# Kernel tuning notes

Hardware: AMD Instinct MI355X
Metric: run time of the kernel (lower is better)

The kernel has to match this reference:

```python
import jax, jax.numpy as jnp
import numpy as np

D_MODEL = 2048
NUM_HEADS = 16
HEAD_DIM = 128
BATCH = 4
SEQ = 2048


def setup_inputs() -> dict:
    key = jax.random.key(0)
    ks = jax.random.split(key, 5)
    s = 0.02
    return {
        "x": jax.random.normal(ks[0], (BATCH, SEQ, D_MODEL), dtype=jnp.float32),
        "Wq": jax.random.normal(ks[1], (NUM_HEADS * HEAD_DIM, D_MODEL), dtype=jnp.float32) * s,
        "Wk": jax.random.normal(ks[2], (NUM_HEADS * HEAD_DIM, D_MODEL), dtype=jnp.float32) * s,
        "Wv": jax.random.normal(ks[3], (NUM_HEADS * HEAD_DIM, D_MODEL), dtype=jnp.float32) * s,
        "Wo": jax.random.normal(ks[4], (D_MODEL, NUM_HEADS * HEAD_DIM), dtype=jnp.float32) * s,
    }


def _split_heads(t):
    b, s, _ = t.shape
    return t.reshape(b, s, NUM_HEADS, HEAD_DIM).transpose(0, 2, 1, 3)  # [b,h,s,d]


def reference(x, Wq, Wk, Wv, Wo):
    # prefill: QKV proj + causal SDPA + output proj. torch Linear: x @ W.T
    q = _split_heads(x @ Wq.T)
    k = _split_heads(x @ Wk.T)
    v = _split_heads(x @ Wv.T)
    scale = 1.0 / jnp.sqrt(jnp.asarray(HEAD_DIM, dtype=x.dtype))
    scores = jnp.einsum("bhqd,bhkd->bhqk", q, k) * scale
    causal = jnp.tril(jnp.ones((SEQ, SEQ), dtype=bool))
    scores = jnp.where(causal, scores, jnp.finfo(scores.dtype).min)
    attn = jax.nn.softmax(scores, axis=-1)
    y = jnp.einsum("bhqk,bhkd->bhqd", attn, v)
    y = y.transpose(0, 2, 1, 3).reshape(x.shape[0], SEQ, NUM_HEADS * HEAD_DIM)
    y = y @ Wo.T
    return (y, k, v)
```

## Files before the change

### kernel.cpp

```cpp
#include <hip/hip_runtime.h>
#include <stdint.h>

#define DM 2048
#define NH 16
#define HD 128
#define BB 4
#define SS 2048
#define BS (BB*SS)
#define NQKV (3*DM)
#define SCQ 0.12751744565f

typedef __bf16 bf16_t;
typedef __attribute__((ext_vector_type(8))) __bf16 bf16x8;
typedef __attribute__((ext_vector_type(4))) float f32x4;
typedef __attribute__((ext_vector_type(16))) float f32x16;
typedef __attribute__((ext_vector_type(4))) float float4v;
typedef __attribute__((ext_vector_type(4))) unsigned int uint4v;
typedef __attribute__((ext_vector_type(4))) unsigned short ushort4v;
typedef __attribute__((ext_vector_type(8))) unsigned short ushort8;

__device__ __forceinline__ unsigned short f2bf(float f) {
  unsigned u = __float_as_uint(f);
  u += 0x7fffu + ((u >> 16) & 1u);
  return (unsigned short)(u >> 16);
}

__device__ __forceinline__ void gl16(const void* g, void* l) {
  __builtin_amdgcn_global_load_lds(
      (const __attribute__((address_space(1))) unsigned int*)(unsigned long long)g,
      (__attribute__((address_space(3))) unsigned int*)(unsigned int)(unsigned long long)l,
      16, 0, 0);
}

__global__ void conv_f32_bf16(const float* __restrict__ in,
                              unsigned short* __restrict__ out, int n4) {
  int i = blockIdx.x * blockDim.x + threadIdx.x;
  int stride = gridDim.x * blockDim.x;
  for (; i < n4; i += stride) {
    float4v v = ((const float4v*)in)[i];
    ushort4v o;
    o.x = f2bf(v.x); o.y = f2bf(v.y); o.z = f2bf(v.z); o.w = f2bf(v.w);
    ((ushort4v*)out)[i] = o;
  }
}

template<int MODE>
__global__ __launch_bounds__(512)
void gemm256(const bf16_t* __restrict__ A, const bf16_t* __restrict__ Bm,
             const int K, const int N, const int nbx,
             float* __restrict__ Cf, bf16_t* __restrict__ qbf,
             bf16_t* __restrict__ kbt, float* __restrict__ kf,
             float* __restrict__ vf, bf16_t* __restrict__ vtb) {
  __shared__ bf16_t As[4][256 * 32];
  __shared__ bf16_t Bs[4][256 * 32];
  const int t = threadIdx.x, w = t >> 6, lane = t & 63;
  const int fr = lane & 15, fq = lane >> 4;
  const int cpx = gridDim.x >> 3;
  const int orig = blockIdx.x;
  const int wg = (orig & 7) * cpx + (orig >> 3);
  const int bm = wg % nbx, bn = wg / nbx;
  const int row0 = bm * 256, col0 = bn * 256;
  const int wm = (w >> 2) * 128, wn = (w & 3) * 64;

  const int i0 = t, i1 = 512 + t;
  const int r0 = i0 >> 2, c0 = i0 & 3;
  const int r1 = i1 >> 2, c1 = i1 & 3;
  const bf16_t* A0 = A + (size_t)(row0 + r0) * K + ((c0 ^ ((r0 >> 1) & 3)) * 8);
  const bf16_t* A1 = A + (size_t)(row0 + r1) * K + ((c1 ^ ((r1 >> 1) & 3)) * 8);
  const bf16_t* B0 = Bm + (size_t)(col0 + r0) * K + ((c0 ^ ((r0 >> 1) & 3)) * 8);
  const bf16_t* B1 = Bm + (size_t)(col0 + r1) * K + ((c1 ^ ((r1 >> 1) & 3)) * 8);

  const int NT = K >> 5;
  f32x4 acc[8][4] = {};

#define STAGE(TT)                                                      \
  {                                                                    \
    const int sl_ = (TT) & 3;                                          \
    const size_t ko_ = (size_t)(TT) * 32;                              \
    gl16(A0 + ko_, (char*)(&As[sl_][0]) + w * 1024);                   \
    gl16(A1 + ko_, (char*)(&As[sl_][0]) + 8192 + w * 1024);            \
    gl16(B0 + ko_, (char*)(&Bs[sl_][0]) + w * 1024);                   \
    gl16(B1 + ko_, (char*)(&Bs[sl_][0]) + 8192 + w * 1024);            \
  }

  STAGE(0); STAGE(1); STAGE(2);

  for (int T = 0; T < NT; ++T) {
    if (T + 3 < NT) {
      STAGE(T + 3);
      asm volatile("s_waitcnt vmcnt(12)" ::: "memory");
    } else if (T + 3 == NT) {
      asm volatile("s_waitcnt vmcnt(8)" ::: "memory");
    } else if (T + 2 == NT) {
      asm volatile("s_waitcnt vmcnt(4)" ::: "memory");
    } else {
      asm volatile("s_waitcnt vmcnt(0)" ::: "memory");
    }
    asm volatile("s_barrier" ::: "memory");

    const bf16_t* al = &As[T & 3][0];
    const bf16_t* bl = &Bs[T & 3][0];
    bf16x8 bfv[4];
#pragma unroll
    for (int n = 0; n < 4; ++n) {
      int rb = wn + n * 16 + fr;
      bfv[n] = *(const bf16x8*)(bl + rb * 32 + ((fq ^ ((rb >> 1) & 3)) * 8));
    }
    __builtin_amdgcn_s_setprio(1);
#pragma unroll
    for (int f = 0; f < 8; ++f) {
      int ra = wm + f * 16 + fr;
      bf16x8 af = *(const bf16x8*)(al + ra * 32 + ((fq ^ ((ra >> 1) & 3)) * 8));
#pragma unroll
      for (int n = 0; n < 4; ++n)
        acc[f][n] = __builtin_amdgcn_mfma_f32_16x16x32_bf16(af, bfv[n], acc[f][n], 0, 0, 0);
    }
    __builtin_amdgcn_s_setprio(0);
    asm volatile("s_barrier" ::: "memory");
  }
#undef STAGE

#pragma unroll
  for (int f = 0; f < 8; ++f) {
#pragma unroll
    for (int jn = 0; jn < 4; ++jn) {
#pragma unroll
      for (int r = 0; r < 4; ++r) {
        int m = row0 + wm + f * 16 + fq * 4 + r;
        int n = col0 + wn + jn * 16 + fr;
        float v = acc[f][jn][r];
        if (MODE == 0) {
          Cf[(size_t)m * N + n] = v;
        } else {
          int b = m >> 11, s = m & 2047;
          if (n < DM) {
            int h = n >> 7, d = n & 127;
            qbf[(((size_t)(b * NH + h)) * SS + s) * HD + d] = (bf16_t)(v * SCQ);
          } else if (n < 2 * DM) {
            int nn = n - DM, h = nn >> 7, d = nn & 127;
            size_t o = (((size_t)(b * NH + h)) * SS + s) * HD + d;
            kbt[o] = (bf16_t)v;
            kf[o] = v;
          } else {
            int nn = n - 2 * DM, h = nn >> 7, d = nn & 127;
            size_t o = (((size_t)(b * NH + h)) * SS + s) * HD + d;
            vf[o] = v;
            vtb[((size_t)(b * NH + h)) * (HD * SS) + (size_t)d * SS + s] = (bf16_t)v;
          }
        }
      }
    }
  }
}

__global__ __launch_bounds__(256, 2)
void attn_fwd4(const bf16_t* __restrict__ qbf, const bf16_t* __restrict__ kbf,
               const bf16_t* __restrict__ vt, bf16_t* __restrict__ aout) {
  __shared__ bf16_t Ks[2][64 * 128];
  __shared__ bf16_t Vs[2][64 * 128];
  const int t = threadIdx.x, w = t >> 6, lane = t & 63;
  const int l31 = lane & 31, hi = lane >> 5;
  const int orig = blockIdx.x;
  const int wg = (orig & 7) * 128 + (orig >> 3);
  const int bh = wg >> 4;
  const int qt = 15 - (wg & 15);
  const int q0 = qt * 128;
  const int nt = 2 * qt + 2;
  const size_t bh_off = (size_t)bh * SS * HD;
  const char* kbase = (const char*)(kbf + bh_off);
  const char* vbase = (const char*)(vt + bh_off);

  const char* ksrc[4];
  const char* vsrc[4];
#pragma unroll
  for (int i = 0; i < 4; ++i) {
    int r = (w * 4 + i) * 4 + (lane >> 4);
    int c = (lane & 15) ^ (r & 15);
    ksrc[i] = kbase + r * 256 + c * 16;
    int d = 2 * r + (c >> 3);
    vsrc[i] = vbase + (size_t)d * (SS * 2) + (c & 7) * 16;
  }

  bf16x8 qfr[8];
  {
    const char* qrow = (const char*)(qbf + bh_off + (size_t)(q0 + w * 32 + l31) * HD);
#pragma unroll
    for (int ds = 0; ds < 8; ++ds)
      qfr[ds] = *(const bf16x8*)(qrow + ds * 32 + hi * 16);
  }

#pragma unroll
  for (int i = 0; i < 4; ++i) {
    gl16(ksrc[i], (char*)(&Ks[0][0]) + (w * 4 + i) * 1024);
    gl16(vsrc[i], (char*)(&Vs[0][0]) + (w * 4 + i) * 1024);
    ksrc[i] += 16384;
    vsrc[i] += 128;
  }

  float mrow = -3.0e38f, lrow = 0.f;
  f32x16 accO[4] = {};

  auto make_pa = [&](const f32x16& sv, bf16x8& paA, bf16x8& paB) {
    unsigned W[8];
#pragma unroll
    for (int m = 0; m < 8; ++m) {
      float lo = sv[2 * m], hh = sv[2 * m + 1];
      asm("v_cvt_pk_bf16_f32 %0, %1, %2" : "=v"(W[m]) : "v"(lo), "v"(hh));
    }
#pragma unroll
    for (int g = 0; g < 2; ++g) {
      unsigned A = W[4 * g], B = W[4 * g + 1], C = W[4 * g + 2], D = W[4 * g + 3];
      unsigned xA = (unsigned)__shfl_xor((int)A, 32, 64);
      unsigned xB = (unsigned)__shfl_xor((int)B, 32, 64);
      unsigned xC = (unsigned)__shfl_xor((int)C, 32, 64);
      unsigned xD = (unsigned)__shfl_xor((int)D, 32, 64);
      uint4v u;
      u.x = hi ? xC : A;
      u.y = hi ? xD : B;
      u.z = hi ? C : xA;
      u.w = hi ? D : xB;
      if (g == 0) paA = __builtin_bit_cast(bf16x8, u);
      else        paB = __builtin_bit_cast(bf16x8, u);
    }
  };

  for (int kt = 0; kt < nt; ++kt) {
    const int cur = kt & 1;
    __syncthreads();

    if (kt + 1 < nt) {
#pragma unroll
      for (int i = 0; i < 4; ++i) {
        gl16(ksrc[i], (char*)(&Ks[cur ^ 1][0]) + (w * 4 + i) * 1024);
        gl16(vsrc[i], (char*)(&Vs[cur ^ 1][0]) + (w * 4 + i) * 1024);
        ksrc[i] += 16384;
        vsrc[i] += 128;
      }
    }

    const char* kl = (const char*)&Ks[cur][0];
    f32x16 s0 = {}, s1 = {};
    const int rck = l31 & 15;
    __builtin_amdgcn_s_setprio(1);
#pragma unroll
    for (int ds = 0; ds < 8; ++ds) {
      int ch = ((2 * ds + hi) ^ rck) << 4;
      bf16x8 kf0 = *(const bf16x8*)(kl + l31 * 256 + ch);
      s0 = __builtin_amdgcn_mfma_f32_32x32x16_bf16(kf0, qfr[ds], s0, 0, 0, 0);
      bf16x8 kf1 = *(const bf16x8*)(kl + (32 + l31) * 256 + ch);
      s1 = __builtin_amdgcn_mfma_f32_32x32x16_bf16(kf1, qfr[ds], s1, 0, 0, 0);
    }
    __builtin_amdgcn_s_setprio(0);

    const int kv0 = kt * 64;
    if (kt >= 2 * qt) {
      const int qg = q0 + w * 32 + l31;
#pragma unroll
      for (int r = 0; r < 16; ++r) {
        int klo = kv0 + (r & 3) + 8 * (r >> 2) + 4 * hi;
        if (klo > qg) s0[r] = -3.0e38f;
        if (klo + 32 > qg) s1[r] = -3.0e38f;
      }
    }
    float rm = s0[0];
#pragma unroll
    for (int r = 1; r < 16; ++r) rm = fmaxf(rm, s0[r]);
#pragma unroll
    for (int r = 0; r < 16; ++r) rm = fmaxf(rm, s1[r]);
    rm = fmaxf(rm, __shfl_xor(rm, 32, 64));
    if (__ballot(rm > mrow + 8.0f)) {
      float mnew = fmaxf(mrow, rm);
      float fct = __builtin_amdgcn_exp2f(mrow - mnew);
      mrow = mnew;
      lrow *= fct;
#pragma unroll
      for (int r = 0; r < 16; ++r) {
        float f = __shfl(fct, (r & 3) + 8 * (r >> 2) + 4 * hi, 64);
        accO[0][r] *= f; accO[1][r] *= f; accO[2][r] *= f; accO[3][r] *= f;
      }
    }
    float ss = 0.f;
#pragma unroll
    for (int r = 0; r < 16; ++r) { float p = __builtin_amdgcn_exp2f(s0[r] - mrow); s0[r] = p; ss += p; }
#pragma unroll
    for (int r = 0; r < 16; ++r) { float p = __builtin_amdgcn_exp2f(s1[r] - mrow); s1[r] = p; ss += p; }
    ss += __shfl_xor(ss, 32, 64);
    lrow += ss;

    bf16x8 pa00, pa01, pa10, pa11;
    make_pa(s0, pa00, pa01);
    make_pa(s1, pa10, pa11);

    const char* vl = (const char*)&Vs[cur][0];
    __builtin_amdgcn_s_setprio(1);
#pragma unroll
    for (int dt = 0; dt < 4; ++dt) {
      int R = dt * 16 + (l31 >> 1);
      int cb = (l31 & 1) << 3;
      int rx = R & 15;
      bf16x8 v00 = *(const bf16x8*)(vl + R * 256 + (((cb + 0 + hi) ^ rx) << 4));
      accO[dt] = __builtin_amdgcn_mfma_f32_32x32x16_bf16(pa00, v00, accO[dt], 0, 0, 0);
      bf16x8 v01 = *(const bf16x8*)(vl + R * 256 + (((cb + 2 + hi) ^ rx) << 4));
      accO[dt] = __builtin_amdgcn_mfma_f32_32x32x16_bf16(pa01, v01, accO[dt], 0, 0, 0);
      bf16x8 v10 = *(const bf16x8*)(vl + R * 256 + (((cb + 4 + hi) ^ rx) << 4));
      accO[dt] = __builtin_amdgcn_mfma_f32_32x32x16_bf16(pa10, v10, accO[dt], 0, 0, 0);
      bf16x8 v11 = *(const bf16x8*)(vl + R * 256 + (((cb + 6 + hi) ^ rx) << 4));
      accO[dt] = __builtin_amdgcn_mfma_f32_32x32x16_bf16(pa11, v11, accO[dt], 0, 0, 0);
    }
    __builtin_amdgcn_s_setprio(0);
  }

  const int b = bh >> 4, h = bh & 15;
#pragma unroll
  for (int r = 0; r < 16; ++r) {
    int qr = (r & 3) + 8 * (r >> 2) + 4 * hi;
    float inv = __builtin_amdgcn_rcpf(__shfl(lrow, qr, 64));
    int srow = q0 + w * 32 + qr;
    bf16_t* orow = aout + ((size_t)(b * SS + srow)) * DM + h * HD + l31;
    orow[0]  = (bf16_t)(accO[0][r] * inv);
    orow[32] = (bf16_t)(accO[1][r] * inv);
    orow[64] = (bf16_t)(accO[2][r] * inv);
    orow[96] = (bf16_t)(accO[3][r] * inv);
  }
}

extern "C" void kernel_launch(void* const* d_in, const int* in_sizes, int n_in,
                              void* d_out, int out_size, void* d_ws, size_t ws_size,
                              hipStream_t stream) {
  (void)in_sizes; (void)n_in; (void)out_size; (void)ws_size;
  const float* x  = (const float*)d_in[0];
  const float* Wq = (const float*)d_in[1];
  const float* Wk = (const float*)d_in[2];
  const float* Wv = (const float*)d_in[3];
  const float* Wo = (const float*)d_in[4];

  float* y  = (float*)d_out;
  float* kf = y + (size_t)BS * DM;
  float* vf = kf + (size_t)BS * DM;

  char* ws = (char*)d_ws;
  bf16_t* xbf  = (bf16_t*)ws;
  bf16_t* abf  = xbf;
  bf16_t* qbf  = (bf16_t*)(ws + (size_t)32 * 1024 * 1024);
  bf16_t* wobf = qbf;
  bf16_t* wqkv = (bf16_t*)(ws + (size_t)64 * 1024 * 1024);
  bf16_t* kbt  = (bf16_t*)y;
  bf16_t* vtb  = (bf16_t*)((char*)y + (size_t)32 * 1024 * 1024);

  conv_f32_bf16<<<2048, 256, 0, stream>>>(x, (unsigned short*)xbf, BS * DM / 4);
  conv_f32_bf16<<<512, 256, 0, stream>>>(Wq, (unsigned short*)wqkv, DM * DM / 4);
  conv_f32_bf16<<<512, 256, 0, stream>>>(Wk, (unsigned short*)(wqkv + (size_t)DM * DM), DM * DM / 4);
  conv_f32_bf16<<<512, 256, 0, stream>>>(Wv, (unsigned short*)(wqkv + 2 * (size_t)DM * DM), DM * DM / 4);

  gemm256<1><<<768, 512, 0, stream>>>(
      xbf, wqkv, DM, NQKV, 32, nullptr, qbf, kbt, kf, vf, vtb);

  attn_fwd4<<<1024, 256, 0, stream>>>(qbf, kbt, vtb, abf);

  conv_f32_bf16<<<512, 256, 0, stream>>>(Wo, (unsigned short*)wobf, DM * DM / 4);

  gemm256<0><<<256, 512, 0, stream>>>(
      abf, wobf, DM, DM, 32, y, nullptr, nullptr, nullptr, nullptr, nullptr);
}
```

Before: 529.3 us.

## Restructure GEMM into double-buffered K=64 tiles with ping-pong barrier phases

Replaces the 4-stage, K=32 LDS pipeline of the 256x256 GEMM with a 2-buffer, K=64 pipeline using an 8-row XOR swizzle. The main loop is split into four sub-phases separated by barriers, and the B-tile prefetch is deferred to the second phase. This aims to halve the outer-loop barrier count per K and interleave warp scheduling, ping-pong style, so loads overlap MFMA work. LDS use stays at 128KB, but prefetch depth drops to a single stage, so memory latency may be less well hidden.

```diff
diff --git a/kernel.cpp b/kernel.cpp
--- a/kernel.cpp
+++ b/kernel.cpp
@@ -46,13 +46,13 @@
 
 template<int MODE>
 __global__ __launch_bounds__(512)
-void gemm256(const bf16_t* __restrict__ A, const bf16_t* __restrict__ Bm,
-             const int K, const int N, const int nbx,
-             float* __restrict__ Cf, bf16_t* __restrict__ qbf,
-             bf16_t* __restrict__ kbt, float* __restrict__ kf,
-             float* __restrict__ vf, bf16_t* __restrict__ vtb) {
-  __shared__ bf16_t As[4][256 * 32];
-  __shared__ bf16_t Bs[4][256 * 32];
+void gemm8p(const bf16_t* __restrict__ A, const bf16_t* __restrict__ Bm,
+            const int K, const int N, const int nbx,
+            float* __restrict__ Cf, bf16_t* __restrict__ qbf,
+            bf16_t* __restrict__ kbt, float* __restrict__ kf,
+            float* __restrict__ vf, bf16_t* __restrict__ vtb) {
+  __shared__ bf16_t As[2][256 * 64];
+  __shared__ bf16_t Bs[2][256 * 64];
   const int t = threadIdx.x, w = t >> 6, lane = t & 63;
   const int fr = lane & 15, fq = lane >> 4;
   const int cpx = gridDim.x >> 3;
@@ -62,63 +62,126 @@
   const int row0 = bm * 256, col0 = bn * 256;
   const int wm = (w >> 2) * 128, wn = (w & 3) * 64;
 
-  const int i0 = t, i1 = 512 + t;
-  const int r0 = i0 >> 2, c0 = i0 & 3;
-  const int r1 = i1 >> 2, c1 = i1 & 3;
-  const bf16_t* A0 = A + (size_t)(row0 + r0) * K + ((c0 ^ ((r0 >> 1) & 3)) * 8);
-  const bf16_t* A1 = A + (size_t)(row0 + r1) * K + ((c1 ^ ((r1 >> 1) & 3)) * 8);
-  const bf16_t* B0 = Bm + (size_t)(col0 + r0) * K + ((c0 ^ ((r0 >> 1) & 3)) * 8);
-  const bf16_t* B1 = Bm + (size_t)(col0 + r1) * K + ((c1 ^ ((r1 >> 1) & 3)) * 8);
-
-  const int NT = K >> 5;
+  const bf16_t* Asrc[4];
+  const bf16_t* Bsrc[4];
+  int dst[4];
+#pragma unroll
+  for (int j = 0; j < 4; ++j) {
+    int u = j * 512 + t, r = u >> 3, c = u & 7;
+    Asrc[j] = A + (size_t)(row0 + r) * K + ((c ^ (r & 7)) * 8);
+    Bsrc[j] = Bm + (size_t)(col0 + r) * K + ((c ^ (r & 7)) * 8);
+    dst[j] = u * 16;
+  }
+  const int NT = K >> 6;
   f32x4 acc[8][4] = {};
 
-#define STAGE(TT)                                                      \
-  {                                                                    \
-    const int sl_ = (TT) & 3;                                          \
-    const size_t ko_ = (size_t)(TT) * 32;                              \
-    gl16(A0 + ko_, (char*)(&As[sl_][0]) + w * 1024);                   \
-    gl16(A1 + ko_, (char*)(&As[sl_][0]) + 8192 + w * 1024);            \
-    gl16(B0 + ko_, (char*)(&Bs[sl_][0]) + w * 1024);                   \
-    gl16(B1 + ko_, (char*)(&Bs[sl_][0]) + 8192 + w * 1024);            \
-  }
-
-  STAGE(0); STAGE(1); STAGE(2);
+#pragma unroll
+  for (int j = 0; j < 4; ++j) gl16(Asrc[j], (char*)(&As[0][0]) + dst[j]);
+#pragma unroll
+  for (int j = 0; j < 4; ++j) gl16(Bsrc[j], (char*)(&Bs[0][0]) + dst[j]);
 
   for (int T = 0; T < NT; ++T) {
-    if (T + 3 < NT) {
-      STAGE(T + 3);
-      asm volatile("s_waitcnt vmcnt(12)" ::: "memory");
-    } else if (T + 3 == NT) {
-      asm volatile("s_waitcnt vmcnt(8)" ::: "memory");
-    } else if (T + 2 == NT) {
+    const bf16_t* al = &As[T & 1][0];
+    const bf16_t* bl = &Bs[T & 1][0];
+    char* Ad = (char*)(&As[(T & 1) ^ 1][0]);
+    char* Bd = (char*)(&Bs[(T & 1) ^ 1][0]);
+    const size_t ko = (size_t)(T + 1) * 64;
+
+    if (T + 1 < NT) {
+#pragma unroll
+      for (int j = 0; j < 4; ++j) gl16(Asrc[j] + ko, Ad + dst[j]);
       asm volatile("s_waitcnt vmcnt(4)" ::: "memory");
     } else {
       asm volatile("s_waitcnt vmcnt(0)" ::: "memory");
     }
     asm volatile("s_barrier" ::: "memory");
 
-    const bf16_t* al = &As[T & 3][0];
-    const bf16_t* bl = &Bs[T & 3][0];
-    bf16x8 bfv[4];
+    auto LDA = [&](int f, int ks) {
+      int ra = wm + f * 16 + fr;
+      return *(const bf16x8*)(al + ra * 64 + (((fq + ks * 4) ^ (ra & 7)) * 8));
+    };
+
+    bf16x8 bfv[4][2];
 #pragma unroll
     for (int n = 0; n < 4; ++n) {
       int rb = wn + n * 16 + fr;
-      bfv[n] = *(const bf16x8*)(bl + rb * 32 + ((fq ^ ((rb >> 1) & 3)) * 8));
-    }
-    __builtin_amdgcn_s_setprio(1);
-#pragma unroll
-    for (int f = 0; f < 8; ++f) {
-      int ra = wm + f * 16 + fr;
-      bf16x8 af = *(const bf16x8*)(al + ra * 32 + ((fq ^ ((ra >> 1) & 3)) * 8));
-#pragma unroll
-      for (int n = 0; n < 4; ++n)
-        acc[f][n] = __builtin_amdgcn_mfma_f32_16x16x32_bf16(af, bfv[n], acc[f][n], 0, 0, 0);
-    }
-    __builtin_amdgcn_s_setprio(0);
-    asm volatile("s_barrier" ::: "memory");
-  }
-#undef STAGE
+#pragma unroll
+      for (int ks = 0; ks < 2; ++ks)
+        bfv[n][ks] = *(const bf16x8*)(bl + rb * 64 + (((fq + ks * 4) ^ (rb & 7)) * 8));
+    }
+    {
+      bf16x8 a00 = LDA(0, 0), a01 = LDA(0, 1), a10 = LDA(1, 0), a11 = LDA(1, 1);
+      __builtin_amdgcn_s_barrier();
+      __builtin_amdgcn_s_setprio(1);
+#pragma unroll
+      for (int n = 0; n < 4; ++n) {
+        acc[0][n] = __builtin_amdgcn_mfma_f32_16x16x32_bf16(a00, bfv[n][0], acc[0][n], 0, 0, 0);
+        acc[1][n] = __builtin_amdgcn_mfma_f32_16x16x32_bf16(a10, bfv[n][0], acc[1][n], 0, 0, 0);
+      }
+#pragma unroll
+      for (int n = 0; n < 4; ++n) {
+        acc[0][n] = __builtin_amdgcn_mfma_f32_16x16x32_bf16(a01, bfv[n][1], acc[0][n], 0, 0, 0);
+        acc[1][n] = __builtin_amdgcn_mfma_f32_16x16x32_bf16(a11, bfv[n][1], acc[1][n], 0, 0, 0);
+      }
+      __builtin_amdgcn_s_setprio(0);
+      __builtin_amdgcn_s_barrier();
+    }
+    {
+      bf16x8 a00 = LDA(2, 0), a01 = LDA(2, 1), a10 = LDA(3, 0), a11 = LDA(3, 1);
+      if (T + 1 < NT) {
+#pragma unroll
+        for (int j = 0; j < 4; ++j) gl16(Bsrc[j] + ko, Bd + dst[j]);
+      }
+      __builtin_amdgcn_s_barrier();
+      __builtin_amdgcn_s_setprio(1);
+#pragma unroll
+      for (int n = 0; n < 4; ++n) {
+        acc[2][n] = __builtin_amdgcn_mfma_f32_16x16x32_bf16(a00, bfv[n][0], acc[2][n], 0, 0, 0);
+        acc[3][n] = __builtin_amdgcn_mfma_f32_16x16x32_bf16(a10, bfv[n][0], acc[3][n], 0, 0, 0);
+      }
+#pragma unroll
+      for (int n = 0; n < 4; ++n) {
+        acc[2][n] = __builtin_amdgcn_mfma_f32_16x16x32_bf16(a01, bfv[n][1], acc[2][n], 0, 0, 0);
+        acc[3][n] = __builtin_amdgcn_mfma_f32_16x16x32_bf16(a11, bfv[n][1], acc[3][n], 0, 0, 0);
+      }
+      __builtin_amdgcn_s_setprio(0);
+      __builtin_amdgcn_s_barrier();
+    }
+    {
+      bf16x8 a00 = LDA(4, 0), a01 = LDA(4, 1), a10 = LDA(5, 0), a11 = LDA(5, 1);
+      __builtin_amdgcn_s_barrier();
+      __builtin_amdgcn_s_setprio(1);
+#pragma unroll
+      for (int n = 0; n < 4; ++n) {
+        acc[4][n] = __builtin_amdgcn_mfma_f32_16x16x32_bf16(a00, bfv[n][0], acc[4][n], 0, 0, 0);
+        acc[5][n] = __builtin_amdgcn_mfma_f32_16x16x32_bf16(a10, bfv[n][0], acc[5][n], 0, 0, 0);
+      }
+#pragma unroll
+      for (int n = 0; n < 4; ++n) {
+        acc[4][n] = __builtin_amdgcn_mfma_f32_16x16x32_bf16(a01, bfv[n][1], acc[4][n], 0, 0, 0);
+        acc[5][n] = __builtin_amdgcn_mfma_f32_16x16x32_bf16(a11, bfv[n][1], acc[5][n], 0, 0, 0);
+      }
+      __builtin_amdgcn_s_setprio(0);
+      __builtin_amdgcn_s_barrier();
+    }
+    {
+      bf16x8 a00 = LDA(6, 0), a01 = LDA(6, 1), a10 = LDA(7, 0), a11 = LDA(7, 1);
+      __builtin_amdgcn_s_barrier();
+      __builtin_amdgcn_s_setprio(1);
+#pragma unroll
+      for (int n = 0; n < 4; ++n) {
+        acc[6][n] = __builtin_amdgcn_mfma_f32_16x16x32_bf16(a00, bfv[n][0], acc[6][n], 0, 0, 0);
+        acc[7][n] = __builtin_amdgcn_mfma_f32_16x16x32_bf16(a10, bfv[n][0], acc[7][n], 0, 0, 0);
+      }
+#pragma unroll
+      for (int n = 0; n < 4; ++n) {
+        acc[6][n] = __builtin_amdgcn_mfma_f32_16x16x32_bf16(a01, bfv[n][1], acc[6][n], 0, 0, 0);
+        acc[7][n] = __builtin_amdgcn_mfma_f32_16x16x32_bf16(a11, bfv[n][1], acc[7][n], 0, 0, 0);
+      }
+      __builtin_amdgcn_s_setprio(0);
+      __builtin_amdgcn_s_barrier();
+    }
+  }
 
 #pragma unroll
   for (int f = 0; f < 8; ++f) {
@@ -352,13 +415,13 @@
   conv_f32_bf16<<<512, 256, 0, stream>>>(Wk, (unsigned short*)(wqkv + (size_t)DM * DM), DM * DM / 4);
   conv_f32_bf16<<<512, 256, 0, stream>>>(Wv, (unsigned short*)(wqkv + 2 * (size_t)DM * DM), DM * DM / 4);
 
-  gemm256<1><<<768, 512, 0, stream>>>(
+  gemm8p<1><<<768, 512, 0, stream>>>(
       xbf, wqkv, DM, NQKV, 32, nullptr, qbf, kbt, kf, vf, vtb);
 
   attn_fwd4<<<1024, 256, 0, stream>>>(qbf, kbt, vtb, abf);
 
   conv_f32_bf16<<<512, 256, 0, stream>>>(Wo, (unsigned short*)wobf, DM * DM / 4);
 
-  gemm256<0><<<256, 512, 0, stream>>>(
+  gemm8p<0><<<256, 512, 0, stream>>>(
       abf, wobf, DM, DM, 32, y, nullptr, nullptr, nullptr, nullptr, nullptr);
 }
```

Measured after the change: 510.3 us. 1.04x faster.

## Restructure GEMM to 64-deep K tiles with double buffering and interleaved phases

Applied to the files above, without the earlier changes.

Replaces the 4-stage, K=32 LDS pipeline in both GEMMs with a 2-stage, K=64 double buffer. The global-to-LDS loads for the next tile are split across MFMA phases, and LDS reads are issued as inline ds_read_b128 with immediate offsets under an 8-way XOR swizzle. The aim is fewer barriers per unit of K, global loads that overlap compute, and less address arithmetic. In exchange it adds more barriers per iteration and has only one tile of prefetch depth, so global latency may be exposed.

```diff
diff --git a/kernel.cpp b/kernel.cpp
--- a/kernel.cpp
+++ b/kernel.cpp
@@ -31,6 +31,9 @@
       (__attribute__((address_space(3))) unsigned int*)(unsigned int)(unsigned long long)l,
       16, 0, 0);
 }
+
+#define DSR(dst, addr, IMM)                                                   \
+  asm volatile("ds_read_b128 %0, %1 offset:" IMM : "=v"(dst) : "v"(addr))
 
 __global__ void conv_f32_bf16(const float* __restrict__ in,
                               unsigned short* __restrict__ out, int n4) {
@@ -46,13 +49,13 @@
 
 template<int MODE>
 __global__ __launch_bounds__(512)
-void gemm256(const bf16_t* __restrict__ A, const bf16_t* __restrict__ Bm,
-             const int K, const int N, const int nbx,
-             float* __restrict__ Cf, bf16_t* __restrict__ qbf,
-             bf16_t* __restrict__ kbt, float* __restrict__ kf,
-             float* __restrict__ vf, bf16_t* __restrict__ vtb) {
-  __shared__ bf16_t As[4][256 * 32];
-  __shared__ bf16_t Bs[4][256 * 32];
+void gemm8a(const bf16_t* __restrict__ A, const bf16_t* __restrict__ Bm,
+            const int K, const int N, const int nbx,
+            float* __restrict__ Cf, bf16_t* __restrict__ qbf,
+            bf16_t* __restrict__ kbt, float* __restrict__ kf,
+            float* __restrict__ vf, bf16_t* __restrict__ vtb) {
+  __shared__ bf16_t As[2][256 * 64];
+  __shared__ bf16_t Bs[2][256 * 64];
   const int t = threadIdx.x, w = t >> 6, lane = t & 63;
   const int fr = lane & 15, fq = lane >> 4;
   const int cpx = gridDim.x >> 3;
@@ -62,63 +65,109 @@
   const int row0 = bm * 256, col0 = bn * 256;
   const int wm = (w >> 2) * 128, wn = (w & 3) * 64;
 
-  const int i0 = t, i1 = 512 + t;
-  const int r0 = i0 >> 2, c0 = i0 & 3;
-  const int r1 = i1 >> 2, c1 = i1 & 3;
-  const bf16_t* A0 = A + (size_t)(row0 + r0) * K + ((c0 ^ ((r0 >> 1) & 3)) * 8);
-  const bf16_t* A1 = A + (size_t)(row0 + r1) * K + ((c1 ^ ((r1 >> 1) & 3)) * 8);
-  const bf16_t* B0 = Bm + (size_t)(col0 + r0) * K + ((c0 ^ ((r0 >> 1) & 3)) * 8);
-  const bf16_t* B1 = Bm + (size_t)(col0 + r1) * K + ((c1 ^ ((r1 >> 1) & 3)) * 8);
-
-  const int NT = K >> 5;
+  const bf16_t* Asrc[4];
+  const bf16_t* Bsrc[4];
+  int dst[4];
+#pragma unroll
+  for (int j = 0; j < 4; ++j) {
+    int u = j * 512 + t, r = u >> 3, c = u & 7;
+    Asrc[j] = A + (size_t)(row0 + r) * K + ((c ^ (r & 7)) * 8);
+    Bsrc[j] = Bm + (size_t)(col0 + r) * K + ((c ^ (r & 7)) * 8);
+    dst[j] = u * 16;
+  }
+  const int NT = K >> 6;
   f32x4 acc[8][4] = {};
 
-#define STAGE(TT)                                                      \
-  {                                                                    \
-    const int sl_ = (TT) & 3;                                          \
-    const size_t ko_ = (size_t)(TT) * 32;                              \
-    gl16(A0 + ko_, (char*)(&As[sl_][0]) + w * 1024);                   \
-    gl16(A1 + ko_, (char*)(&As[sl_][0]) + 8192 + w * 1024);            \
-    gl16(B0 + ko_, (char*)(&Bs[sl_][0]) + w * 1024);                   \
-    gl16(B1 + ko_, (char*)(&Bs[sl_][0]) + 8192 + w * 1024);            \
-  }
-
-  STAGE(0); STAGE(1); STAGE(2);
+  const unsigned As0 = (unsigned)(unsigned long long)(const void*)&As[0][0];
+  const unsigned Bs0 = (unsigned)(unsigned long long)(const void*)&Bs[0][0];
+  const unsigned arow = (unsigned)(wm + fr) * 128;
+  const unsigned brow = (unsigned)(wn + fr) * 128;
+  const unsigned x0 = (unsigned)((fq ^ (fr & 7)) * 16);
+  const unsigned x1 = (unsigned)(((fq + 4) ^ (fr & 7)) * 16);
+
+#pragma unroll
+  for (int j = 0; j < 4; ++j) gl16(Asrc[j], (char*)(&As[0][0]) + dst[j]);
+#pragma unroll
+  for (int j = 0; j < 4; ++j) gl16(Bsrc[j], (char*)(&Bs[0][0]) + dst[j]);
+  asm volatile("s_waitcnt vmcnt(0)" ::: "memory");
+  asm volatile("s_barrier" ::: "memory");
+
+#define MFMA_PAIR(F0, F1)                                                     \
+  __builtin_amdgcn_s_setprio(1);                                              \
+  _Pragma("unroll")                                                           \
+  for (int n = 0; n < 4; ++n) {                                               \
+    acc[F0][n] = __builtin_amdgcn_mfma_f32_16x16x32_bf16(                     \
+        __builtin_bit_cast(bf16x8, q00), __builtin_bit_cast(bf16x8, bfv[n][0]), acc[F0][n], 0, 0, 0); \
+    acc[F1][n] = __builtin_amdgcn_mfma_f32_16x16x32_bf16(                     \
+        __builtin_bit_cast(bf16x8, q10), __builtin_bit_cast(bf16x8, bfv[n][0]), acc[F1][n], 0, 0, 0); \
+  }                                                                           \
+  _Pragma("unroll")                                                           \
+  for (int n = 0; n < 4; ++n) {                                               \
+    acc[F0][n] = __builtin_amdgcn_mfma_f32_16x16x32_bf16(                     \
+        __builtin_bit_cast(bf16x8, q01), __builtin_bit_cast(bf16x8, bfv[n][1]), acc[F0][n], 0, 0, 0); \
+    acc[F1][n] = __builtin_amdgcn_mfma_f32_16x16x32_bf16(                     \
+        __builtin_bit_cast(bf16x8, q11), __builtin_bit_cast(bf16x8, bfv[n][1]), acc[F1][n], 0, 0, 0); \
+  }                                                                           \
+  __builtin_amdgcn_s_setprio(0);
 
   for (int T = 0; T < NT; ++T) {
-    if (T + 3 < NT) {
-      STAGE(T + 3);
-      asm volatile("s_waitcnt vmcnt(12)" ::: "memory");
-    } else if (T + 3 == NT) {
-      asm volatile("s_waitcnt vmcnt(8)" ::: "memory");
-    } else if (T + 2 == NT) {
-      asm volatile("s_waitcnt vmcnt(4)" ::: "memory");
-    } else {
-      asm volatile("s_waitcnt vmcnt(0)" ::: "memory");
-    }
-    asm volatile("s_barrier" ::: "memory");
-
-    const bf16_t* al = &As[T & 3][0];
-    const bf16_t* bl = &Bs[T & 3][0];
-    bf16x8 bfv[4];
-#pragma unroll
-    for (int n = 0; n < 4; ++n) {
-      int rb = wn + n * 16 + fr;
-      bfv[n] = *(const bf16x8*)(bl + rb * 32 + ((fq ^ ((rb >> 1) & 3)) * 8));
-    }
-    __builtin_amdgcn_s_setprio(1);
-#pragma unroll
-    for (int f = 0; f < 8; ++f) {
-      int ra = wm + f * 16 + fr;
-      bf16x8 af = *(const bf16x8*)(al + ra * 32 + ((fq ^ ((ra >> 1) & 3)) * 8));
-#pragma unroll
-      for (int n = 0; n < 4; ++n)
-        acc[f][n] = __builtin_amdgcn_mfma_f32_16x16x32_bf16(af, bfv[n], acc[f][n], 0, 0, 0);
-    }
-    __builtin_amdgcn_s_setprio(0);
-    asm volatile("s_barrier" ::: "memory");
-  }
-#undef STAGE
+    char* Ad = (char*)(&As[(T & 1) ^ 1][0]);
+    char* Bd = (char*)(&Bs[(T & 1) ^ 1][0]);
+    const size_t ko = (size_t)(T + 1) * 64;
+    const unsigned ab = As0 + (unsigned)(T & 1) * 32768;
+    const unsigned bb = Bs0 + (unsigned)(T & 1) * 32768;
+    const unsigned a0 = ab + arow + x0, a1 = ab + arow + x1;
+    const unsigned b0 = bb + brow + x0, b1 = bb + brow + x1;
+
+    uint4v bfv[4][2];
+    uint4v q00, q01, q10, q11;
+
+    DSR(bfv[0][0], b0, "0");    DSR(bfv[0][1], b1, "0");
+    DSR(bfv[1][0], b0, "2048"); DSR(bfv[1][1], b1, "2048");
+    DSR(bfv[2][0], b0, "4096"); DSR(bfv[2][1], b1, "4096");
+    DSR(bfv[3][0], b0, "6144"); DSR(bfv[3][1], b1, "6144");
+    DSR(q00, a0, "0");    DSR(q01, a1, "0");
+    DSR(q10, a0, "2048"); DSR(q11, a1, "2048");
+    if (T + 1 < NT) {
+#pragma unroll
+      for (int j = 0; j < 4; ++j) gl16(Asrc[j] + ko, Ad + dst[j]);
+    }
+    asm volatile("s_barrier" ::: "memory");
+    asm volatile("s_waitcnt lgkmcnt(0)" ::: "memory");
+    __builtin_amdgcn_sched_barrier(0);
+    MFMA_PAIR(0, 1)
+    asm volatile("s_barrier" ::: "memory");
+
+    DSR(q00, a0, "4096"); DSR(q01, a1, "4096");
+    DSR(q10, a0, "6144"); DSR(q11, a1, "6144");
+    if (T + 1 < NT) {
+#pragma unroll
+      for (int j = 0; j < 4; ++j) gl16(Bsrc[j] + ko, Bd + dst[j]);
+    }
+    asm volatile("s_barrier" ::: "memory");
+    asm volatile("s_waitcnt lgkmcnt(0)" ::: "memory");
+    __builtin_amdgcn_sched_barrier(0);
+    MFMA_PAIR(2, 3)
+    asm volatile("s_barrier" ::: "memory");
+
+    DSR(q00, a0, "8192");  DSR(q01, a1, "8192");
+    DSR(q10, a0, "10240"); DSR(q11, a1, "10240");
+    asm volatile("s_barrier" ::: "memory");
+    asm volatile("s_waitcnt lgkmcnt(0)" ::: "memory");
+    __builtin_amdgcn_sched_barrier(0);
+    MFMA_PAIR(4, 5)
+    asm volatile("s_barrier" ::: "memory");
+
+    DSR(q00, a0, "12288"); DSR(q01, a1, "12288");
+    DSR(q10, a0, "14336"); DSR(q11, a1, "14336");
+    asm volatile("s_barrier" ::: "memory");
+    asm volatile("s_waitcnt lgkmcnt(0)" ::: "memory");
+    __builtin_amdgcn_sched_barrier(0);
+    MFMA_PAIR(6, 7)
+    asm volatile("s_waitcnt vmcnt(0)" ::: "memory");
+    asm volatile("s_barrier" ::: "memory");
+  }
+#undef MFMA_PAIR
 
 #pragma unroll
   for (int f = 0; f < 8; ++f) {
@@ -352,13 +401,13 @@
   conv_f32_bf16<<<512, 256, 0, stream>>>(Wk, (unsigned short*)(wqkv + (size_t)DM * DM), DM * DM / 4);
   conv_f32_bf16<<<512, 256, 0, stream>>>(Wv, (unsigned short*)(wqkv + 2 * (size_t)DM * DM), DM * DM / 4);
 
-  gemm256<1><<<768, 512, 0, stream>>>(
+  gemm8a<1><<<768, 512, 0, stream>>>(
       xbf, wqkv, DM, NQKV, 32, nullptr, qbf, kbt, kf, vf, vtb);
 
   attn_fwd4<<<1024, 256, 0, stream>>>(qbf, kbt, vtb, abf);
 
   conv_f32_bf16<<<512, 256, 0, stream>>>(Wo, (unsigned short*)wobf, DM * DM / 4);
 
-  gemm256<0><<<256, 512, 0, stream>>>(
+  gemm8a<0><<<256, 512, 0, stream>>>(
       abf, wobf, DM, DM, 32, y, nullptr, nullptr, nullptr, nullptr, nullptr);
 }
```

Result: faster. 518.7 us (-2.0%).

## Restructure GEMM main loop: single barrier, batched LDS reads, split waits

Applied to the files above, without the earlier changes.

Reworks the bf16 GEMM inner loop so each K-step uses one barrier instead of two. The prefetch for stage T+3 is now issued after the barrier, into the slot that was consumed in the previous iteration. All LDS fragment reads are issued up front as inline ds_read_b128 with immediate offsets. The first half of the MFMAs starts after a partial lgkmcnt wait, which overlaps LDS latency with math. The swizzle pattern also changes to a simpler r&3 XOR. The aim is to cut barrier stalls and LDS address arithmetic, at the cost of fragile hand-written waitcnt bookkeeping.

```diff
diff --git a/kernel.cpp b/kernel.cpp
--- a/kernel.cpp
+++ b/kernel.cpp
@@ -31,6 +31,9 @@
       (__attribute__((address_space(3))) unsigned int*)(unsigned int)(unsigned long long)l,
       16, 0, 0);
 }
+
+#define DSR(dst, addr, IMM)                                                   \
+  asm volatile("ds_read_b128 %0, %1 offset:" IMM : "=v"(dst) : "v"(addr))
 
 __global__ void conv_f32_bf16(const float* __restrict__ in,
                               unsigned short* __restrict__ out, int n4) {
@@ -46,11 +49,11 @@
 
 template<int MODE>
 __global__ __launch_bounds__(512)
-void gemm256(const bf16_t* __restrict__ A, const bf16_t* __restrict__ Bm,
-             const int K, const int N, const int nbx,
-             float* __restrict__ Cf, bf16_t* __restrict__ qbf,
-             bf16_t* __restrict__ kbt, float* __restrict__ kf,
-             float* __restrict__ vf, bf16_t* __restrict__ vtb) {
+void gemmr4(const bf16_t* __restrict__ A, const bf16_t* __restrict__ Bm,
+            const int K, const int N, const int nbx,
+            float* __restrict__ Cf, bf16_t* __restrict__ qbf,
+            bf16_t* __restrict__ kbt, float* __restrict__ kf,
+            float* __restrict__ vf, bf16_t* __restrict__ vtb) {
   __shared__ bf16_t As[4][256 * 32];
   __shared__ bf16_t Bs[4][256 * 32];
   const int t = threadIdx.x, w = t >> 6, lane = t & 63;
@@ -62,63 +65,82 @@
   const int row0 = bm * 256, col0 = bn * 256;
   const int wm = (w >> 2) * 128, wn = (w & 3) * 64;
 
-  const int i0 = t, i1 = 512 + t;
-  const int r0 = i0 >> 2, c0 = i0 & 3;
-  const int r1 = i1 >> 2, c1 = i1 & 3;
-  const bf16_t* A0 = A + (size_t)(row0 + r0) * K + ((c0 ^ ((r0 >> 1) & 3)) * 8);
-  const bf16_t* A1 = A + (size_t)(row0 + r1) * K + ((c1 ^ ((r1 >> 1) & 3)) * 8);
-  const bf16_t* B0 = Bm + (size_t)(col0 + r0) * K + ((c0 ^ ((r0 >> 1) & 3)) * 8);
-  const bf16_t* B1 = Bm + (size_t)(col0 + r1) * K + ((c1 ^ ((r1 >> 1) & 3)) * 8);
-
+  const bf16_t* Asrc[2];
+  const bf16_t* Bsrc[2];
+  int dst[2];
+#pragma unroll
+  for (int j = 0; j < 2; ++j) {
+    int u = j * 512 + t, r = u >> 2, c = u & 3;
+    Asrc[j] = A + (size_t)(row0 + r) * K + ((c ^ (r & 3)) * 8);
+    Bsrc[j] = Bm + (size_t)(col0 + r) * K + ((c ^ (r & 3)) * 8);
+    dst[j] = u * 16;
+  }
   const int NT = K >> 5;
   f32x4 acc[8][4] = {};
 
-#define STAGE(TT)                                                      \
-  {                                                                    \
-    const int sl_ = (TT) & 3;                                          \
-    const size_t ko_ = (size_t)(TT) * 32;                              \
-    gl16(A0 + ko_, (char*)(&As[sl_][0]) + w * 1024);                   \
-    gl16(A1 + ko_, (char*)(&As[sl_][0]) + 8192 + w * 1024);            \
-    gl16(B0 + ko_, (char*)(&Bs[sl_][0]) + w * 1024);                   \
-    gl16(B1 + ko_, (char*)(&Bs[sl_][0]) + 8192 + w * 1024);            \
-  }
+  const unsigned As0 = (unsigned)(unsigned long long)(const void*)&As[0][0];
+  const unsigned Bs0 = (unsigned)(unsigned long long)(const void*)&Bs[0][0];
+  const unsigned xorc = (unsigned)((fq ^ (fr & 3)) << 4);
+  const unsigned aoff = (unsigned)((wm + fr) * 64) + xorc;
+  const unsigned boff = (unsigned)((wn + fr) * 64) + xorc;
+
+#define STAGE(TT)                                                  \
+  {                                                                \
+    const int sl_ = (TT) & 3;                                      \
+    const size_t ko_ = (size_t)(TT) * 32;                          \
+    gl16(Asrc[0] + ko_, (char*)(&As[sl_][0]) + dst[0]);            \
+    gl16(Asrc[1] + ko_, (char*)(&As[sl_][0]) + dst[1]);            \
+    gl16(Bsrc[0] + ko_, (char*)(&Bs[sl_][0]) + dst[0]);            \
+    gl16(Bsrc[1] + ko_, (char*)(&Bs[sl_][0]) + dst[1]);            \
+  }
+
+#define MFQUAD(FI, AV)                                                        \
+  acc[FI][0] = __builtin_amdgcn_mfma_f32_16x16x32_bf16(                       \
+      __builtin_bit_cast(bf16x8, AV), __builtin_bit_cast(bf16x8, bv0), acc[FI][0], 0, 0, 0); \
+  acc[FI][1] = __builtin_amdgcn_mfma_f32_16x16x32_bf16(                       \
+      __builtin_bit_cast(bf16x8, AV), __builtin_bit_cast(bf16x8, bv1), acc[FI][1], 0, 0, 0); \
+  acc[FI][2] = __builtin_amdgcn_mfma_f32_16x16x32_bf16(                       \
+      __builtin_bit_cast(bf16x8, AV), __builtin_bit_cast(bf16x8, bv2), acc[FI][2], 0, 0, 0); \
+  acc[FI][3] = __builtin_amdgcn_mfma_f32_16x16x32_bf16(                       \
+      __builtin_bit_cast(bf16x8, AV), __builtin_bit_cast(bf16x8, bv3), acc[FI][3], 0, 0, 0);
 
   STAGE(0); STAGE(1); STAGE(2);
 
   for (int T = 0; T < NT; ++T) {
-    if (T + 3 < NT) {
-      STAGE(T + 3);
-      asm volatile("s_waitcnt vmcnt(12)" ::: "memory");
-    } else if (T + 3 == NT) {
+    if (T + 2 < NT) {
       asm volatile("s_waitcnt vmcnt(8)" ::: "memory");
-    } else if (T + 2 == NT) {
+    } else if (T + 1 < NT) {
       asm volatile("s_waitcnt vmcnt(4)" ::: "memory");
     } else {
       asm volatile("s_waitcnt vmcnt(0)" ::: "memory");
     }
     asm volatile("s_barrier" ::: "memory");
-
-    const bf16_t* al = &As[T & 3][0];
-    const bf16_t* bl = &Bs[T & 3][0];
-    bf16x8 bfv[4];
-#pragma unroll
-    for (int n = 0; n < 4; ++n) {
-      int rb = wn + n * 16 + fr;
-      bfv[n] = *(const bf16x8*)(bl + rb * 32 + ((fq ^ ((rb >> 1) & 3)) * 8));
-    }
+    if (T + 3 < NT) STAGE(T + 3);
+
+    const unsigned ab = As0 + (unsigned)(T & 3) * 16384 + aoff;
+    const unsigned bb = Bs0 + (unsigned)(T & 3) * 16384 + boff;
+    uint4v bv0, bv1, bv2, bv3, a0, a1, a2, a3, a4, a5, a6, a7;
+    DSR(bv0, bb, "0");    DSR(bv1, bb, "1024");
+    DSR(bv2, bb, "2048"); DSR(bv3, bb, "3072");
+    DSR(a0, ab, "0");     DSR(a1, ab, "1024");
+    DSR(a2, ab, "2048");  DSR(a3, ab, "3072");
+    DSR(a4, ab, "4096");  DSR(a5, ab, "5120");
+    DSR(a6, ab, "6144");  DSR(a7, ab, "7168");
+
+    asm volatile("s_waitcnt lgkmcnt(4)" ::: "memory");
+    __builtin_amdgcn_sched_barrier(0);
     __builtin_amdgcn_s_setprio(1);
-#pragma unroll
-    for (int f = 0; f < 8; ++f) {
-      int ra = wm + f * 16 + fr;
-      bf16x8 af = *(const bf16x8*)(al + ra * 32 + ((fq ^ ((ra >> 1) & 3)) * 8));
-#pragma unroll
-      for (int n = 0; n < 4; ++n)
-        acc[f][n] = __builtin_amdgcn_mfma_f32_16x16x32_bf16(af, bfv[n], acc[f][n], 0, 0, 0);
-    }
+    MFQUAD(0, a0) MFQUAD(1, a1) MFQUAD(2, a2) MFQUAD(3, a3)
     __builtin_amdgcn_s_setprio(0);
-    asm volatile("s_barrier" ::: "memory");
+
+    asm volatile("s_waitcnt lgkmcnt(0)" ::: "memory");
+    __builtin_amdgcn_sched_barrier(0);
+    __builtin_amdgcn_s_setprio(1);
+    MFQUAD(4, a4) MFQUAD(5, a5) MFQUAD(6, a6) MFQUAD(7, a7)
+    __builtin_amdgcn_s_setprio(0);
   }
 #undef STAGE
+#undef MFQUAD
 
 #pragma unroll
   for (int f = 0; f < 8; ++f) {
@@ -352,13 +374,13 @@
   conv_f32_bf16<<<512, 256, 0, stream>>>(Wk, (unsigned short*)(wqkv + (size_t)DM * DM), DM * DM / 4);
   conv_f32_bf16<<<512, 256, 0, stream>>>(Wv, (unsigned short*)(wqkv + 2 * (size_t)DM * DM), DM * DM / 4);
 
-  gemm256<1><<<768, 512, 0, stream>>>(
+  gemmr4<1><<<768, 512, 0, stream>>>(
       xbf, wqkv, DM, NQKV, 32, nullptr, qbf, kbt, kf, vf, vtb);
 
   attn_fwd4<<<1024, 256, 0, stream>>>(qbf, kbt, vtb, abf);
 
   conv_f32_bf16<<<512, 256, 0, stream>>>(Wo, (unsigned short*)wobf, DM * DM / 4);
 
-  gemm256<0><<<256, 512, 0, stream>>>(
+  gemmr4<0><<<256, 512, 0, stream>>>(
       abf, wobf, DM, DM, 32, y, nullptr, nullptr, nullptr, nullptr, nullptr);
 }
```

Result: no change. 520.0 us (-1.8%).
